# Optimization experiments

Measured on AMD Instinct MI355X. Metric: run time of the kernel, lower is better.

Reference implementation:

```python
import jax, jax.numpy as jnp
import numpy as np

INPUT_SIZE = 64


def _xavier(key, shape):
    fan_in, fan_out = shape[1], shape[0]
    bound = float(np.sqrt(6.0 / (fan_in + fan_out)))
    return jax.random.uniform(key, shape, jnp.float32, -bound, bound)


def setup_inputs() -> dict:
    key = jax.random.key(0)
    k_x, k_wih, k_whh, k_wout = jax.random.split(key, 4)
    B, N, F = 32768, 16, INPUT_SIZE + 1
    inputs = jax.random.normal(k_x, (B, N, F), jnp.float32)
    # GRU(input_size, hidden=1): weight_ih [3*1, input_size], weight_hh [3*1, 1]
    W_ih = _xavier(k_wih, (3, INPUT_SIZE))
    W_hh = _xavier(k_whh, (3, 1))
    b_ih = jnp.zeros((3,), jnp.float32)
    b_hh = jnp.zeros((3,), jnp.float32)
    # Linear(1, 1)
    w_out = _xavier(k_wout, (1, 1))
    b_out = jnp.zeros((1,), jnp.float32)
    return {"inputs": inputs, "W_ih": W_ih, "W_hh": W_hh, "b_ih": b_ih,
            "b_hh": b_hh, "w_out": w_out, "b_out": b_out}


def reference(inputs, W_ih, W_hh, b_ih, b_hh, w_out, b_out):
    B, N, F = inputs.shape
    x = inputs[..., 1:].reshape(B * N, F - 1)   # GRU input, one timestep
    h = inputs[..., :1].reshape(B * N, 1)       # initial hidden state
    # Single GRU cell step (PyTorch gate ordering: r, z, n)
    gi = x @ W_ih.T + b_ih                      # [BN, 3]
    gh = h @ W_hh.T + b_hh                      # [BN, 3]
    r = jax.nn.sigmoid(gi[:, 0:1] + gh[:, 0:1])
    z = jax.nn.sigmoid(gi[:, 1:2] + gh[:, 1:2])
    n = jnp.tanh(gi[:, 2:3] + r * gh[:, 2:3])
    h_new = (1.0 - z) * n + z * h               # [BN, 1]
    out = h_new * w_out[0, 0] + b_out[0]        # Linear(1,1)
    return out.reshape(B, N, 1)
```

## Files before the change

kernel.cpp:

```cpp
#include <hip/hip_runtime.h>
#include <math.h>


#define THREADS 64
#define RPB 64
#define ROW_F 65
#define REGION_F (RPB * ROW_F)
#define FULL_ITERS 16
#define TAIL_F4 16

__device__ __forceinline__ float sigmoidf_(float v) {
    return 1.0f / (1.0f + __expf(-v));
}

__device__ __forceinline__ void async_copy16(const void* g, void* l) {
    __builtin_amdgcn_global_load_lds(
        (const __attribute__((address_space(1))) void*)g,
        (__attribute__((address_space(3))) void*)l,
        16, 0, 0);
}

__global__ __launch_bounds__(THREADS)
void gru_cell_kernel(const float* __restrict__ inputs,
                     const float* __restrict__ W_ih,
                     const float* __restrict__ W_hh,
                     const float* __restrict__ b_ih,
                     const float* __restrict__ b_hh,
                     const float* __restrict__ w_out,
                     const float* __restrict__ b_out,
                     float* __restrict__ out)
{
    __shared__ float  ldsRow[REGION_F];
    __shared__ float4 ldsW4[48];

    const int lane = threadIdx.x;
    const size_t base = (size_t)blockIdx.x * REGION_F;
    const char* gsrc = (const char*)(inputs + base);

    #pragma unroll
    for (int it = 0; it < FULL_ITERS; ++it) {
        async_copy16(gsrc + it * 1024 + lane * 16,
                     (char*)ldsRow + it * 1024);
    }
    if (lane < TAIL_F4) {
        reinterpret_cast<float4*>(ldsRow)[FULL_ITERS * 64 + lane] =
            reinterpret_cast<const float4*>(gsrc)[FULL_ITERS * 64 + lane];
    }
    if (lane < 48) {
        ldsW4[lane] = reinterpret_cast<const float4*>(W_ih)[lane];
    }

    __syncthreads();

    const float* row = ldsRow + lane * ROW_F;
    const float h = row[0];
    const float* x = row + 1;

    float a0 = 0.0f, a1 = 0.0f, a2 = 0.0f;
    #pragma unroll
    for (int j4 = 0; j4 < 16; ++j4) {
        const float4 w0 = ldsW4[j4];
        const float4 w1 = ldsW4[16 + j4];
        const float4 w2 = ldsW4[32 + j4];
        const float x0 = x[4 * j4 + 0];
        const float x1 = x[4 * j4 + 1];
        const float x2 = x[4 * j4 + 2];
        const float x3 = x[4 * j4 + 3];
        a0 = fmaf(x0, w0.x, a0); a0 = fmaf(x1, w0.y, a0);
        a0 = fmaf(x2, w0.z, a0); a0 = fmaf(x3, w0.w, a0);
        a1 = fmaf(x0, w1.x, a1); a1 = fmaf(x1, w1.y, a1);
        a1 = fmaf(x2, w1.z, a1); a1 = fmaf(x3, w1.w, a1);
        a2 = fmaf(x0, w2.x, a2); a2 = fmaf(x1, w2.y, a2);
        a2 = fmaf(x2, w2.z, a2); a2 = fmaf(x3, w2.w, a2);
    }

    const float gh0 = fmaf(h, W_hh[0], b_hh[0]);
    const float gh1 = fmaf(h, W_hh[1], b_hh[1]);
    const float gh2 = fmaf(h, W_hh[2], b_hh[2]);

    const float r = sigmoidf_(a0 + b_ih[0] + gh0);
    const float z = sigmoidf_(a1 + b_ih[1] + gh1);
    const float n = tanhf(a2 + b_ih[2] + r * gh2);
    const float h_new = (1.0f - z) * n + z * h;

    out[(size_t)blockIdx.x * RPB + lane] = fmaf(h_new, w_out[0], b_out[0]);
}

extern "C" void kernel_launch(void* const* d_in, const int* in_sizes, int n_in,
                              void* d_out, int out_size, void* d_ws, size_t ws_size,
                              hipStream_t stream) {
    const float* inputs = (const float*)d_in[0];
    const float* W_ih   = (const float*)d_in[1];
    const float* W_hh   = (const float*)d_in[2];
    const float* b_ih   = (const float*)d_in[3];
    const float* b_hh   = (const float*)d_in[4];
    const float* w_out  = (const float*)d_in[5];
    const float* b_out  = (const float*)d_in[6];
    float* out = (float*)d_out;

    const int nrows  = in_sizes[0] / ROW_F;
    const int blocks = nrows / RPB;

    gru_cell_kernel<<<dim3(blocks), dim3(THREADS), 0, stream>>>(
        inputs, W_ih, W_hh, b_ih, b_hh, w_out, b_out, out);
}
```

Measured before the change: 26.71 us.

## Split each row's dot product across four lanes with shuffle reduction

Each row's 64-wide dot products are now split across 4 threads, each handling 16 features, with xor-shuffle reductions. Blocks grow to 128 threads covering 32 rows, which doubles the block count and shortens each thread's serial FMA chain. The async LDS copy is reorganised for two waves with a per-wave LDS offset. In exchange, three lanes per row do redundant gate math and stay idle at the store, and LDS reads of x now stride across rows, which may cause bank conflicts.

Measured after the change: 26.21 us. Within noise of the previous version (-1.9%).

```diff
diff --git a/kernel.cpp b/kernel.cpp
--- a/kernel.cpp
+++ b/kernel.cpp
@@ -2,12 +2,13 @@
 #include <math.h>
 
 
-#define THREADS 64
-#define RPB 64
+#define THREADS 128
+#define RPB 32
 #define ROW_F 65
 #define REGION_F (RPB * ROW_F)
-#define FULL_ITERS 16
-#define TAIL_F4 16
+#define REGION_B (REGION_F * 4)
+#define FULL_ITERS 4
+#define TAIL_F4 8
 
 __device__ __forceinline__ float sigmoidf_(float v) {
     return 1.0f / (1.0f + __expf(-v));
@@ -30,60 +31,63 @@
                      const float* __restrict__ b_out,
                      float* __restrict__ out)
 {
-    __shared__ float  ldsRow[REGION_F];
-    __shared__ float4 ldsW4[48];
+    __shared__ float ldsRow[REGION_F];
+    __shared__ float ldsW[192];
 
-    const int lane = threadIdx.x;
+    const int tid  = threadIdx.x;
     const size_t base = (size_t)blockIdx.x * REGION_F;
     const char* gsrc = (const char*)(inputs + base);
 
+    const int wave_off = (tid >> 6) << 10;
     #pragma unroll
     for (int it = 0; it < FULL_ITERS; ++it) {
-        async_copy16(gsrc + it * 1024 + lane * 16,
-                     (char*)ldsRow + it * 1024);
+        async_copy16(gsrc + it * 2048 + tid * 16,
+                     (char*)ldsRow + it * 2048 + wave_off);
     }
-    if (lane < TAIL_F4) {
-        reinterpret_cast<float4*>(ldsRow)[FULL_ITERS * 64 + lane] =
-            reinterpret_cast<const float4*>(gsrc)[FULL_ITERS * 64 + lane];
+    if (tid < TAIL_F4) {
+        reinterpret_cast<float4*>(ldsRow)[FULL_ITERS * 128 + tid] =
+            reinterpret_cast<const float4*>(gsrc)[FULL_ITERS * 128 + tid];
     }
-    if (lane < 48) {
-        ldsW4[lane] = reinterpret_cast<const float4*>(W_ih)[lane];
+    if (tid < 48) {
+        reinterpret_cast<float4*>(ldsW)[tid] =
+            reinterpret_cast<const float4*>(W_ih)[tid];
     }
 
     __syncthreads();
 
-    const float* row = ldsRow + lane * ROW_F;
-    const float h = row[0];
-    const float* x = row + 1;
+    const int r = tid >> 2;
+    const int q = tid & 3;
+    const float* x  = ldsRow + r * ROW_F + 1 + q * 16;
+    const float* w0 = ldsW +   0 + q * 16;
+    const float* w1 = ldsW +  64 + q * 16;
+    const float* w2 = ldsW + 128 + q * 16;
 
     float a0 = 0.0f, a1 = 0.0f, a2 = 0.0f;
     #pragma unroll
-    for (int j4 = 0; j4 < 16; ++j4) {
-        const float4 w0 = ldsW4[j4];
-        const float4 w1 = ldsW4[16 + j4];
-        const float4 w2 = ldsW4[32 + j4];
-        const float x0 = x[4 * j4 + 0];
-        const float x1 = x[4 * j4 + 1];
-        const float x2 = x[4 * j4 + 2];
-        const float x3 = x[4 * j4 + 3];
-        a0 = fmaf(x0, w0.x, a0); a0 = fmaf(x1, w0.y, a0);
-        a0 = fmaf(x2, w0.z, a0); a0 = fmaf(x3, w0.w, a0);
-        a1 = fmaf(x0, w1.x, a1); a1 = fmaf(x1, w1.y, a1);
-        a1 = fmaf(x2, w1.z, a1); a1 = fmaf(x3, w1.w, a1);
-        a2 = fmaf(x0, w2.x, a2); a2 = fmaf(x1, w2.y, a2);
-        a2 = fmaf(x2, w2.z, a2); a2 = fmaf(x3, w2.w, a2);
+    for (int j = 0; j < 16; ++j) {
+        const float xv = x[j];
+        a0 = fmaf(xv, w0[j], a0);
+        a1 = fmaf(xv, w1[j], a1);
+        a2 = fmaf(xv, w2[j], a2);
     }
 
+    a0 += __shfl_xor(a0, 1); a0 += __shfl_xor(a0, 2);
+    a1 += __shfl_xor(a1, 1); a1 += __shfl_xor(a1, 2);
+    a2 += __shfl_xor(a2, 1); a2 += __shfl_xor(a2, 2);
+
+    const float h = ldsRow[r * ROW_F];
     const float gh0 = fmaf(h, W_hh[0], b_hh[0]);
     const float gh1 = fmaf(h, W_hh[1], b_hh[1]);
     const float gh2 = fmaf(h, W_hh[2], b_hh[2]);
 
-    const float r = sigmoidf_(a0 + b_ih[0] + gh0);
-    const float z = sigmoidf_(a1 + b_ih[1] + gh1);
-    const float n = tanhf(a2 + b_ih[2] + r * gh2);
-    const float h_new = (1.0f - z) * n + z * h;
+    const float rg = sigmoidf_(a0 + b_ih[0] + gh0);
+    const float zg = sigmoidf_(a1 + b_ih[1] + gh1);
+    const float ng = tanhf(a2 + b_ih[2] + rg * gh2);
+    const float h_new = (1.0f - zg) * ng + zg * h;
 
-    out[(size_t)blockIdx.x * RPB + lane] = fmaf(h_new, w_out[0], b_out[0]);
+    if (q == 0) {
+        out[(size_t)blockIdx.x * RPB + r] = fmaf(h_new, w_out[0], b_out[0]);
+    }
 }
 
 extern "C" void kernel_launch(void* const* d_in, const int* in_sizes, int n_in,
```
